# Kernel optimization log

Hardware: AMD Instinct MI355X
Metric: run time of the kernel (lower is better)

## Reference

```python
import jax, jax.numpy as jnp
import numpy as np

B, L, D = 8, 2048, 512


def setup_inputs() -> dict:
    key = jax.random.key(0)
    ks = jax.random.split(key, 9)
    s = 1.0 / np.sqrt(D)
    x = jax.random.normal(ks[0], (B, L, D), dtype=jnp.float32)
    Wq = jax.random.uniform(ks[1], (D, D), jnp.float32, -s, s)
    bq = jax.random.uniform(ks[2], (D,), jnp.float32, -s, s)
    Wk = jax.random.uniform(ks[3], (D, D), jnp.float32, -s, s)
    bk = jax.random.uniform(ks[4], (D,), jnp.float32, -s, s)
    Wv = jax.random.uniform(ks[5], (D, D), jnp.float32, -s, s)
    bv = jax.random.uniform(ks[6], (D,), jnp.float32, -s, s)
    Wo = jax.random.uniform(ks[7], (D, D), jnp.float32, -s, s)
    bo = jax.random.uniform(ks[8], (D,), jnp.float32, -s, s)
    return {"x": x, "Wq": Wq, "bq": bq, "Wk": Wk, "bk": bk,
            "Wv": Wv, "bv": bv, "Wo": Wo, "bo": bo}


def reference(x, Wq, bq, Wk, bk, Wv, bv, Wo, bo):
    # Projections then rfft along sequence axis -> complex [B, F, D], F = L//2+1
    Q = jnp.fft.rfft(x @ Wq + bq, axis=1)
    K = jnp.fft.rfft(x @ Wk + bk, axis=1)
    V = jnp.fft.rfft(x @ Wv + bv, axis=1)
    scale = K.shape[-1] ** (-0.5)
    # Complex attention scores over frequency bins: [B, F, F]
    att = jnp.einsum('bfd,bgd->bfg', Q, K) * scale
    attn = jax.nn.softmax(jnp.abs(att), axis=-1)
    context = jnp.einsum('bfg,bgd->bfd', attn.astype(Q.dtype), V)
    context = jnp.fft.irfft(context, n=x.shape[1], axis=1)  # [B, L, D] real
    return context @ Wo + bo
```

## Files before the change

kernel.cpp:

```cpp
#include <hip/hip_runtime.h>
#include <hip/hip_bf16.h>
#include <math.h>

typedef __hip_bfloat16 bf16;
typedef __attribute__((ext_vector_type(8))) short short8;
typedef __attribute__((ext_vector_type(4))) float f32x4;

#define BB 8
#define LL 2048
#define DD 512
#define FF 1025
#define GP 1088
#define FPAD 1152
#define PSTRIDE 589824
#define ATT_SCALE 0.04419417382415922f

__device__ __forceinline__ float b2f(bf16 v) { return __bfloat162float(v); }
__device__ __forceinline__ bf16  f2b(float v) { return __float2bfloat16(v); }
__device__ __forceinline__ float s2f(short s) { bf16 t; *reinterpret_cast<short*>(&t) = s; return b2f(t); }
__device__ __forceinline__ void splt(float v, short& h, short& l) {
    bf16 hb = f2b(v);
    bf16 lb = f2b(v - b2f(hb));
    h = *reinterpret_cast<short*>(&hb);
    l = *reinterpret_cast<short*>(&lb);
}
__device__ __forceinline__ unsigned pk2(short a, short b) {
    return (unsigned)(unsigned short)a | ((unsigned)(unsigned short)b << 16);
}

#define MFMA16(a, b, c) __builtin_amdgcn_mfma_f32_16x16x32_bf16((a), (b), (c), 0, 0, 0)

__device__ __forceinline__ short8 neg8(short8 v) {
    short8 r;
    #pragma unroll
    for (int t = 0; t < 8; ++t) r[t] = (short)(v[t] ^ (short)0x8000);
    return r;
}

typedef __attribute__((address_space(1))) const unsigned int gu32;
typedef __attribute__((address_space(3))) unsigned int lu32;
__device__ __forceinline__ void gl16(const void* g, void* l) {
    __builtin_amdgcn_global_load_lds((gu32*)g, (lu32*)l, 16, 0, 0);
}

template<bool F32>
__device__ __forceinline__ float ldin(const void* p, size_t i) {
    if (F32) return ((const float*)p)[i];
    else     return b2f(((const bf16*)p)[i]);
}

__global__ __launch_bounds__(256) void detect_dtype(const unsigned short* __restrict__ x,
                                                    int* __restrict__ flag)
{
    __shared__ int cnt[256];
    int c = 0;
    for (int i = threadIdx.x; i < 4096; i += 256) {
        const int e = (x[i] >> 7) & 0xFF;
        c += (e >= 100 && e <= 150) ? 1 : 0;
    }
    cnt[threadIdx.x] = c;
    __syncthreads();
    for (int s = 128; s; s >>= 1) {
        if (threadIdx.x < s) cnt[threadIdx.x] += cnt[threadIdx.x + s];
        __syncthreads();
    }
    if (threadIdx.x == 0) *flag = (cnt[0] < 3400) ? 1 : 0;
}

__global__ __launch_bounds__(256) void prep_bias(const void* __restrict__ b0,
                                                 const void* __restrict__ b1,
                                                 const void* __restrict__ b2,
                                                 const void* __restrict__ b3,
                                                 float* __restrict__ bias_f,
                                                 const int* __restrict__ flag)
{
    const int idx = blockIdx.x * 256 + threadIdx.x;
    const int which = idx >> 9, i = idx & 511;
    const void* src = which == 0 ? b0 : (which == 1 ? b1 : (which == 2 ? b2 : b3));
    bias_f[idx] = (*flag) ? ldin<true>(src, i) : ldin<false>(src, i);
}

__global__ __launch_bounds__(256) void split_w_t(const void* __restrict__ W0,
                                                 const void* __restrict__ W1,
                                                 const void* __restrict__ W2,
                                                 const void* __restrict__ W3,
                                                 bf16* __restrict__ WT,
                                                 const int* __restrict__ flag)
{
    const int z = blockIdx.z;
    const void* W = z == 0 ? W0 : (z == 1 ? W1 : (z == 2 ? W2 : W3));
    bf16* Wh = WT + (size_t)z * 524288;
    bf16* Wl = Wh + 262144;
    const int k0 = blockIdx.x * 32, n0 = blockIdx.y * 32;
    const bool f32 = (*flag) != 0;
    __shared__ float Tl[32][33];
    for (int it = 0; it < 4; ++it) {
        const int idx = it * 256 + threadIdx.x;
        const int lk = idx >> 5, ln = idx & 31;
        Tl[lk][ln] = f32 ? ldin<true>(W, (size_t)(k0 + lk) * 512 + n0 + ln)
                         : ldin<false>(W, (size_t)(k0 + lk) * 512 + n0 + ln);
    }
    __syncthreads();
    for (int it = 0; it < 4; ++it) {
        const int idx = it * 256 + threadIdx.x;
        const int ln = idx >> 5, lk = idx & 31;
        const float v = Tl[lk][ln];
        const bf16 h = f2b(v);
        Wh[(size_t)(n0 + ln) * 512 + k0 + lk] = h;
        Wl[(size_t)(n0 + ln) * 512 + k0 + lk] = f2b(v - b2f(h));
    }
}

__device__ __forceinline__ int shx(int i, int c) {
    const int x = (i << 2) | c;
    return x ^ (((x >> 6) & 3) << 2);
}

__device__ __forceinline__ void fft_decode(int flat, int& b, int& dp) {
    const int c8 = flat & 7;
    const int s  = (flat >> 3) & 1;
    const int pp = flat >> 4;
    const int idx = c8 * 32 + pp;
    b  = idx >> 5;
    dp = ((idx & 31) << 1) | s;
}

__global__ __launch_bounds__(512) void rfft_x(const void* __restrict__ x,
                                              bf16* __restrict__ Xh,
                                              bf16* __restrict__ Xl,
                                              const int* __restrict__ flag)
{
    int b, dp;
    fft_decode(blockIdx.x, b, dp);
    const int d0 = dp * 8;
    __shared__ float2 sh[8192];
    const int tid = threadIdx.x;
    const int c = tid & 3;

    if (*flag) {
        const float* base = (const float*)x + (size_t)b * 2048 * 512 + d0;
        #pragma unroll
        for (int it = 0; it < 8; ++it) {
            const int idx = it * 512 + tid;
            const int l = idx >> 1, fq = idx & 1;
            const float4 v = *(const float4*)(base + (size_t)l * 512 + fq * 4);
            sh[shx(l, fq * 2)]     = make_float2(v.x, v.y);
            sh[shx(l, fq * 2 + 1)] = make_float2(v.z, v.w);
        }
    } else {
        const bf16* base = (const bf16*)x + (size_t)b * 2048 * 512 + d0;
        #pragma unroll
        for (int it = 0; it < 4; ++it) {
            const int l = it * 512 + tid;
            const short8 v = *(const short8*)(base + (size_t)l * 512);
            #pragma unroll
            for (int q = 0; q < 4; ++q)
                sh[shx(l, q)] = make_float2(s2f(v[2 * q]), s2f(v[2 * q + 1]));
        }
    }
    __syncthreads();

    const int jb = tid >> 2;
    #pragma unroll
    for (int lsm = 10; lsm >= 0; --lsm) {
        const int m = 1 << lsm;
        const float step = -3.14159265358979f / (float)m;
        #pragma unroll
        for (int r = 0; r < 8; ++r) {
            const int j  = jb + 128 * r;
            const int k  = j & (m - 1);
            const int i1 = ((j & ~(m - 1)) << 1) | k;
            const int i2 = i1 + m;
            float sw, cw;
            __sincosf(step * (float)k, &sw, &cw);
            const float2 a  = sh[shx(i1, c)];
            const float2 bb = sh[shx(i2, c)];
            sh[shx(i1, c)] = make_float2(a.x + bb.x, a.y + bb.y);
            const float dx = a.x - bb.x, dy = a.y - bb.y;
            sh[shx(i2, c)] = make_float2(dx * cw - dy * sw, dx * sw + dy * cw);
        }
        __syncthreads();
    }

    const int fb = tid >> 2;
    const size_t pan_re = (size_t)(b * 64 + dp) * FPAD;
    const size_t pan_im = pan_re + (size_t)512 * FPAD;
    auto dorow = [&](int f) {
        const int rf = __brev((unsigned)f) >> 21;
        const int rc = __brev((unsigned)((2048 - f) & 2047)) >> 21;
        const float2 Zf = sh[shx(rf, c)];
        const float2 Zc = sh[shx(rc, c)];
        const float x1r = 0.5f * (Zf.x + Zc.x);
        const float x1i = 0.5f * (Zf.y - Zc.y);
        const float x2r = 0.5f * (Zf.y + Zc.y);
        const float x2i = -0.5f * (Zf.x - Zc.x);
        short h1r, l1r, h1i, l1i, h2r, l2r, h2i, l2i;
        splt(x1r, h1r, l1r); splt(x1i, h1i, l1i);
        splt(x2r, h2r, l2r); splt(x2i, h2i, l2i);
        const size_t ro_re = (pan_re + f) * 8 + 2 * c;
        const size_t ro_im = (pan_im + f) * 8 + 2 * c;
        *(unsigned*)&Xh[ro_re] = pk2(h1r, h2r);
        *(unsigned*)&Xh[ro_im] = pk2(h1i, h2i);
        *(unsigned*)&Xl[ro_re] = pk2(l1r, l2r);
        *(unsigned*)&Xl[ro_im] = pk2(l1i, l2i);
    };
    #pragma unroll
    for (int it = 0; it < 8; ++it)
        dorow(fb * 8 + it);
    if (tid < 4) dorow(1024);

    if (tid < 508) {
        const int f = FF + (tid >> 2);
        const int w = tid & 3;
        bf16* basep = (w & 2) ? Xl : Xh;
        const size_t off = (((size_t)((w & 1) * 512 + b * 64 + dp)) * FPAD + f) * 8;
        short8 z = {};
        *(short8*)&basep[off] = z;
    }
}

__global__ __launch_bounds__(256) void proj_all(const bf16* __restrict__ Xh,
                                                const bf16* __restrict__ Xl,
                                                const bf16* __restrict__ WT,
                                                const float* __restrict__ bias_f,
                                                bf16* __restrict__ Q,
                                                bf16* __restrict__ K,
                                                bf16* __restrict__ Vct)
{
    const int flat = blockIdx.x;
    const bool isV = flat < 576;
    int t, ny, z = 0;
    if (isV) { t = flat >> 2; ny = flat & 3; }
    else { const int idx = flat - 576; t = idx >> 3; z = (idx >> 2) & 1; ny = idx & 3; }

    const int pb = t / 9;
    const int f0 = (t - pb * 9) * 128;
    const int plane = pb >> 3, b = pb & 7;
    const int n0 = ny * 128;
    const int tid = threadIdx.x, wv = tid >> 6, lane = tid & 63;
    const int wm = (wv >> 1) * 64, wn = (wv & 1) * 64;
    const size_t pbase = (size_t)pb * PSTRIDE;

    __shared__ __align__(16) bf16 SH[16384];

    const int srow = tid >> 2, sq = tid & 3;
    const int mm = lane & 15, cc = lane >> 4;
    const int rpos = (cc ^ ((mm >> 1) & 3)) * 8;
    const int nn2 = lane & 15, rq = (lane >> 4) * 4;

    if (!isV) {
        const bf16* Bh = WT + (size_t)z * 524288;
        bf16* dst = z == 0 ? Q : K;
        const float* bias = bias_f + z * 512;
        typedef bf16 (*t128)[32];
        t128 Al = (t128)SH;
        t128 Bl = (t128)(SH + 4096);

        f32x4 acc[4][4] = {};
        for (int kt = 0; kt < 512; kt += 32) {
            #pragma unroll
            for (int p = 0; p < 2; ++p) {
                const int r = p * 64 + srow;
                const int pos = (sq ^ ((r >> 1) & 3)) * 8;
                *(uint4*)&Al[r][pos] =
                    *(const uint4*)&Xh[pbase + ((size_t)((kt >> 3) + sq) * FPAD + f0 + r) * 8];
                *(uint4*)&Bl[r][pos] = *(const uint4*)&Bh[(size_t)(n0 + r) * 512 + kt + sq * 8];
            }
            __syncthreads();

            short8 af[4], bfr[4];
            #pragma unroll
            for (int i = 0; i < 4; ++i) {
                af[i]  = *(const short8*)&Al[wm + i * 16 + mm][rpos];
                bfr[i] = *(const short8*)&Bl[wn + i * 16 + mm][rpos];
            }
            #pragma unroll
            for (int i = 0; i < 4; ++i)
                #pragma unroll
                for (int j = 0; j < 4; ++j)
                    acc[i][j] = MFMA16(af[i], bfr[j], acc[i][j]);
            __syncthreads();
        }

        const size_t SPQ = (size_t)BB * FF * DD;
        #pragma unroll
        for (int i = 0; i < 4; ++i)
            #pragma unroll
            for (int j = 0; j < 4; ++j) {
                const int col = n0 + wn + j * 16 + nn2;
                #pragma unroll
                for (int r = 0; r < 4; ++r) {
                    const int f = f0 + wm + i * 16 + rq + r;
                    if (f < FF) {
                        float v = acc[i][j][r];
                        if (plane == 0 && f == 0) v += 2048.0f * bias[col];
                        const int swz = ((f >> 1) & 3) << 3;
                        dst[(size_t)plane * SPQ + ((size_t)(b * FF + f)) * 512 + (col ^ swz)] = f2b(v);
                    }
                }
            }
    } else {
        const bf16* Bh = WT + (size_t)2 * 524288;
        const bf16* Blo = Bh + 262144;
        const float* bias = bias_f + 1024;
        typedef bf16 (*tile_t)[128][32];
        tile_t Al = (tile_t)SH;
        tile_t Bl = (tile_t)(SH + 8192);

        f32x4 acc[4][4] = {};
        for (int kt = 0; kt < 512; kt += 32) {
            #pragma unroll
            for (int p = 0; p < 2; ++p) {
                const int r = p * 64 + srow;
                const int pos = (sq ^ ((r >> 1) & 3)) * 8;
                const size_t aoff = pbase + ((size_t)((kt >> 3) + sq) * FPAD + f0 + r) * 8;
                *(uint4*)&Al[0][r][pos] = *(const uint4*)&Xh[aoff];
                *(uint4*)&Al[1][r][pos] = *(const uint4*)&Xl[aoff];
                *(uint4*)&Bl[0][r][pos] = *(const uint4*)&Bh[(size_t)(n0 + r) * 512 + kt + sq * 8];
                *(uint4*)&Bl[1][r][pos] = *(const uint4*)&Blo[(size_t)(n0 + r) * 512 + kt + sq * 8];
            }
            __syncthreads();

            short8 a_h[4], a_l[4], b_h[4], b_l[4];
            #pragma unroll
            for (int i = 0; i < 4; ++i) {
                a_h[i] = *(const short8*)&Al[0][wm + i * 16 + mm][rpos];
                a_l[i] = *(const short8*)&Al[1][wm + i * 16 + mm][rpos];
                b_h[i] = *(const short8*)&Bl[0][wn + i * 16 + mm][rpos];
                b_l[i] = *(const short8*)&Bl[1][wn + i * 16 + mm][rpos];
            }
            #pragma unroll
            for (int i = 0; i < 4; ++i)
                #pragma unroll
                for (int j = 0; j < 4; ++j) {
                    acc[i][j] = MFMA16(a_h[i], b_h[j], acc[i][j]);
                    acc[i][j] = MFMA16(a_h[i], b_l[j], acc[i][j]);
                    acc[i][j] = MFMA16(a_l[i], b_h[j], acc[i][j]);
                }
            __syncthreads();
        }

        bf16* T = SH;
        #pragma unroll
        for (int i = 0; i < 4; ++i)
            #pragma unroll
            for (int j = 0; j < 4; ++j) {
                const int col_l = wn + j * 16 + nn2;
                #pragma unroll
                for (int r = 0; r < 4; ++r) {
                    const int row_l = wm + i * 16 + rq + r;
                    const int f = f0 + row_l;
                    float v = (f < FF) ? acc[i][j][r] : 0.f;
                    if (plane == 0 && f == 0) v += 2048.0f * bias[n0 + col_l];
                    T[col_l * 128 + (row_l ^ ((col_l & 15) << 3))] = f2b(v);
                }
            }
        __syncthreads();

        const int nl = tid >> 1, half = tid & 1;
        const size_t gbase = ((size_t)(b * 1024 + plane * 512 + n0 + nl)) * GP + f0;
        #pragma unroll
        for (int a = 0; a < 8; ++a) {
            const int fl = half * 64 + a * 8;
            if (f0 + fl < GP) {
                const short8 v8 = *(const short8*)&T[nl * 128 + (fl ^ ((nl & 15) << 3))];
                *(short8*)&Vct[gbase + fl] = v8;
            }
        }
    }
}

__global__ __launch_bounds__(256, 2) void att_mfma(const bf16* __restrict__ Asp,
                                                   const bf16* __restrict__ Bsp,
                                                   float* __restrict__ att)
{
    const size_t SP = (size_t)BB * FF * DD;
    const int flat = blockIdx.x;
    const int b    = flat & 7;
    const int slot = flat >> 3;
    const int grp  = slot / 51;
    const int rem  = slot % 51;
    const int g    = rem / 3;
    const int r3   = rem % 3;
    const int ft   = grp * 3 + r3;
    const int f0 = ft * 128, g0 = g * 64;

    const int tid = threadIdx.x;
    const int wv = tid >> 6, lane = tid & 63;
    const int wvf = wv >> 1, wvg = wv & 1;

    __shared__ __align__(1024) char LB[24576];
    bf16 (*Al)[128][32] = (bf16(*)[128][32])LB;
    bf16 (*Bl)[64][32]  = (bf16(*)[64][32])(LB + 16384);

    f32x4 accr[4][2] = {}; f32x4 acci[4][2] = {};

    const int r16 = lane & 15, cc = lane >> 4;
    const int rpos = (cc ^ ((r16 >> 1) & 3)) * 8;
    const size_t abase = (size_t)(b * FF + f0) * 512;
    const size_t bbase = (size_t)(b * FF + g0) * 512;
    const int lrow = lane >> 2;
    const int lcol = (lane & 3) * 8;

    for (int kt = 0; kt < 512; kt += 32) {
        #pragma unroll
        for (int c2 = 0; c2 < 4; ++c2) {
            const int chunk = wv * 4 + c2;
            const int pl = chunk >> 3, rg = chunk & 7;
            const int row = rg * 16 + lrow;
            gl16(&Asp[(size_t)pl * SP + abase + (size_t)row * 512 + kt + lcol],
                 LB + chunk * 1024);
        }
        #pragma unroll
        for (int c2 = 0; c2 < 2; ++c2) {
            const int chunk = wv * 2 + c2;
            const int pl = chunk >> 2, rg = chunk & 3;
            const int row = rg * 16 + lrow;
            gl16(&Bsp[(size_t)pl * SP + bbase + (size_t)row * 512 + kt + lcol],
                 LB + 16384 + chunk * 1024);
        }
        __syncthreads();

        short8 aA[4][2], bB[2][2], nb[2];
        #pragma unroll
        for (int i = 0; i < 4; ++i) {
            const int row = wvf * 64 + i * 16 + r16;
            #pragma unroll
            for (int pl = 0; pl < 2; ++pl)
                aA[i][pl] = *(const short8*)&Al[pl][row][rpos];
        }
        #pragma unroll
        for (int j = 0; j < 2; ++j) {
            const int row = wvg * 32 + j * 16 + r16;
            #pragma unroll
            for (int pl = 0; pl < 2; ++pl)
                bB[j][pl] = *(const short8*)&Bl[pl][row][rpos];
            nb[j] = neg8(bB[j][1]);
        }
        #pragma unroll
        for (int i = 0; i < 4; ++i)
            #pragma unroll
            for (int j = 0; j < 2; ++j) {
                accr[i][j] = MFMA16(aA[i][0], bB[j][0], accr[i][j]);
                accr[i][j] = MFMA16(aA[i][1], nb[j],    accr[i][j]);
                acci[i][j] = MFMA16(aA[i][0], bB[j][1], acci[i][j]);
                acci[i][j] = MFMA16(aA[i][1], bB[j][0], acci[i][j]);
            }
        __syncthreads();
    }

    const int rq = (lane >> 4) * 4;
    #pragma unroll
    for (int i = 0; i < 4; ++i)
        #pragma unroll
        for (int j = 0; j < 2; ++j)
            #pragma unroll
            for (int r = 0; r < 4; ++r) {
                const int f = f0 + wvf * 64 + i * 16 + rq + r;
                const int gg = g0 + wvg * 32 + j * 16 + r16;
                if (f < FF && gg < FF) {
                    const float ar = accr[i][j][r];
                    const float ai = acci[i][j][r];
                    att[((size_t)(b * FF + f)) * FF + gg] = ATT_SCALE * sqrtf(ar * ar + ai * ai);
                }
            }
}

__global__ __launch_bounds__(256) void softmax_rows(const float* __restrict__ att,
                                                    bf16* __restrict__ att16)
{
    const int row = blockIdx.x;
    const float* p = att + (size_t)row * FF;
    bf16* q = att16 + (size_t)row * GP;
    const int tid = threadIdx.x;
    const int lane = tid & 63, wid = tid >> 6;
    __shared__ float red[4];

    float m = -1e30f;
    for (int i = tid; i < FF; i += 256) m = fmaxf(m, p[i]);
    #pragma unroll
    for (int o = 32; o; o >>= 1) m = fmaxf(m, __shfl_down(m, o));
    if (lane == 0) red[wid] = m;
    __syncthreads();
    m = fmaxf(fmaxf(red[0], red[1]), fmaxf(red[2], red[3]));
    __syncthreads();

    float s = 0.f;
    for (int i = tid; i < FF; i += 256) s += expf(p[i] - m);
    #pragma unroll
    for (int o = 32; o; o >>= 1) s += __shfl_down(s, o);
    if (lane == 0) red[wid] = s;
    __syncthreads();
    s = red[0] + red[1] + red[2] + red[3];
    const float inv = 1.f / s;
    for (int i = tid; i < GP; i += 256)
        q[i] = f2b(i < FF ? expf(p[i] - m) * inv : 0.f);
}

__global__ __launch_bounds__(256, 2) void ctx_mfma(const bf16* __restrict__ att16,
                                                   const bf16* __restrict__ Vct,
                                                   bf16* __restrict__ Csp)
{
    const int flat = blockIdx.x;
    const int b    = flat & 7;
    const int slot = flat >> 3;
    const int ft   = slot >> 4;
    const int nt   = slot & 15;
    const int f0 = ft * 128, n0 = nt * 64;

    const int tid = threadIdx.x;
    const int wv = tid >> 6, lane = tid & 63;
    const int wvf = wv >> 1, wvg = wv & 1;

    __shared__ __align__(16) bf16 Al[128][64];
    __shared__ __align__(16) bf16 Bl[64][64];

    f32x4 acc[4][2] = {};
    const int srow8 = tid >> 3, sq8 = tid & 7;
    const int r16 = lane & 15, cc = lane >> 4;
    const int rpos = (cc ^ ((r16 >> 1) & 3)) * 8;

    for (int kt = 0; kt < GP; kt += 64) {
        #pragma unroll
        for (int p = 0; p < 4; ++p) {
            const int row = p * 32 + srow8;
            const int pos = (sq8 >> 2) * 32 + (((sq8 & 3) ^ ((row >> 1) & 3)) * 8);
            uint4 av = make_uint4(0, 0, 0, 0);
            if (f0 + row < FF)
                av = *(const uint4*)&att16[((size_t)(b * FF + f0 + row)) * GP + kt + sq8 * 8];
            *(uint4*)&Al[row][pos] = av;
        }
        #pragma unroll
        for (int p = 0; p < 2; ++p) {
            const int row = p * 32 + srow8;
            const int pos = (sq8 >> 2) * 32 + (((sq8 & 3) ^ ((row >> 1) & 3)) * 8);
            *(uint4*)&Bl[row][pos] =
                *(const uint4*)&Vct[((size_t)(b * 1024 + n0 + row)) * GP + kt + sq8 * 8];
        }
        __syncthreads();

        #pragma unroll
        for (int kk = 0; kk < 2; ++kk) {
            short8 aA[4], bB[2];
            #pragma unroll
            for (int i = 0; i < 4; ++i)
                aA[i] = *(const short8*)&Al[wvf * 64 + i * 16 + r16][kk * 32 + rpos];
            #pragma unroll
            for (int j = 0; j < 2; ++j)
                bB[j] = *(const short8*)&Bl[wvg * 32 + j * 16 + r16][kk * 32 + rpos];
            #pragma unroll
            for (int i = 0; i < 4; ++i)
                #pragma unroll
                for (int j = 0; j < 2; ++j)
                    acc[i][j] = MFMA16(aA[i], bB[j], acc[i][j]);
        }
        __syncthreads();
    }

    const int rq = (lane >> 4) * 4;
    #pragma unroll
    for (int i = 0; i < 4; ++i)
        #pragma unroll
        for (int j = 0; j < 2; ++j)
            #pragma unroll
            for (int r = 0; r < 4; ++r) {
                const int f = f0 + wvf * 64 + i * 16 + rq + r;
                const int n = n0 + wvg * 32 + j * 16 + r16;
                if (f < FF) {
                    const int d = n & 511, pl = n >> 9;
                    Csp[((size_t)(pl * 8 + b) * FPAD + f) * 512 + d] = f2b(acc[i][j][r]);
                }
            }
}

__global__ __launch_bounds__(256) void out_mfma_freq(const bf16* __restrict__ A,
                                                     const bf16* __restrict__ BhT,
                                                     float* __restrict__ CwR,
                                                     float* __restrict__ CwI)
{
    const int t = blockIdx.x;
    const int pb = t / 9;
    const int f0 = (t - pb * 9) * 128;
    const int plane = pb >> 3, b = pb & 7;
    const int m0 = t * 128, n0 = blockIdx.y * 64;
    const int tid = threadIdx.x, wv = tid >> 6, lane = tid & 63;
    const int wvf = wv >> 1, wvg = wv & 1;

    __shared__ __align__(16) bf16 Al[128][32];
    __shared__ __align__(16) bf16 Bl[64][32];

    f32x4 acc[4][2] = {};
    const int srow = tid >> 2, sq = tid & 3;
    const int r16 = lane & 15, cc = lane >> 4;
    const int rpos = (cc ^ ((r16 >> 1) & 3)) * 8;

    for (int kt = 0; kt < 512; kt += 32) {
        #pragma unroll
        for (int p = 0; p < 2; ++p) {
            const int r = p * 64 + srow;
            const int pos = (sq ^ ((r >> 1) & 3)) * 8;
            *(uint4*)&Al[r][pos] = *(const uint4*)&A[(size_t)(m0 + r) * 512 + kt + sq * 8];
        }
        {
            const int pos = (sq ^ ((srow >> 1) & 3)) * 8;
            *(uint4*)&Bl[srow][pos] = *(const uint4*)&BhT[(size_t)(n0 + srow) * 512 + kt + sq * 8];
        }
        __syncthreads();

        short8 af[4], bfr[2];
        #pragma unroll
        for (int i = 0; i < 4; ++i)
            af[i] = *(const short8*)&Al[wvf * 64 + i * 16 + r16][rpos];
        #pragma unroll
        for (int j = 0; j < 2; ++j)
            bfr[j] = *(const short8*)&Bl[wvg * 32 + j * 16 + r16][rpos];
        #pragma unroll
        for (int i = 0; i < 4; ++i)
            #pragma unroll
            for (int j = 0; j < 2; ++j)
                acc[i][j] = MFMA16(af[i], bfr[j], acc[i][j]);
        __syncthreads();
    }

    float* dst = plane ? CwI : CwR;
    const int nn2 = lane & 15, rq = (lane >> 4) * 4;
    #pragma unroll
    for (int i = 0; i < 4; ++i)
        #pragma unroll
        for (int j = 0; j < 2; ++j) {
            const int col = n0 + wvg * 32 + j * 16 + nn2;
            #pragma unroll
            for (int r = 0; r < 4; ++r) {
                const int f = f0 + wvf * 64 + i * 16 + rq + r;
                if (f < FF)
                    dst[((size_t)(b * FF + f)) * 512 + col] = acc[i][j][r];
            }
        }
}

__global__ __launch_bounds__(512) void irfft8(const float* __restrict__ CwR,
                                              const float* __restrict__ CwI,
                                              void* __restrict__ out,
                                              const float* __restrict__ bias_f,
                                              const int* __restrict__ flag)
{
    int b, dp;
    fft_decode(blockIdx.x, b, dp);
    const int d0 = dp * 8;
    __shared__ float2 sh[8192];
    const int tid = threadIdx.x;
    const int c = tid & 3, fb = tid >> 2;

    for (int it = 0; it < 9; ++it) {
        const int f = fb + 128 * it;
        if (f < FF) {
            const size_t off = ((size_t)(b * FF + f)) * 512 + d0 + 2 * c;
            const float2 vr = *(const float2*)(CwR + off);
            const float2 vi = *(const float2*)(CwI + off);
            float c1x = vr.x, c1y = vi.x, c2x = vr.y, c2y = vi.y;
            if (f == 0 || f == 1024) { c1y = 0.f; c2y = 0.f; }
            sh[shx(f, c)] = make_float2(c1x - c2y, c1y + c2x);
            if (f >= 1 && f <= 1023)
                sh[shx(2048 - f, c)] = make_float2(c1x + c2y, c2x - c1y);
        }
    }
    __syncthreads();

    const int jb = fb;
    #pragma unroll
    for (int lsm = 10; lsm >= 0; --lsm) {
        const int m = 1 << lsm;
        const float step = 3.14159265358979f / (float)m;
        #pragma unroll
        for (int r = 0; r < 8; ++r) {
            const int j  = jb + 128 * r;
            const int k  = j & (m - 1);
            const int i1 = ((j & ~(m - 1)) << 1) | k;
            const int i2 = i1 + m;
            float sw, cw;
            __sincosf(step * (float)k, &sw, &cw);
            const float2 a  = sh[shx(i1, c)];
            const float2 bb = sh[shx(i2, c)];
            sh[shx(i1, c)] = make_float2(a.x + bb.x, a.y + bb.y);
            const float dx = a.x - bb.x, dy = a.y - bb.y;
            sh[shx(i2, c)] = make_float2(dx * cw - dy * sw, dx * sw + dy * cw);
        }
        __syncthreads();
    }

    const float sc = 1.0f / 2048.0f;
    const float bo0 = bias_f[1536 + d0 + 2 * c];
    const float bo1 = bias_f[1536 + d0 + 2 * c + 1];
    const bool f32o = (*flag) != 0;
    const int lb = tid >> 2;
    #pragma unroll
    for (int it = 0; it < 16; ++it) {
        const int l  = lb * 16 + it;
        const int rl = __brev((unsigned)l) >> 21;
        const float2 z = sh[shx(rl, c)];
        const float o0 = z.x * sc + bo0;
        const float o1 = z.y * sc + bo1;
        const size_t off = ((size_t)(b * 2048 + l)) * 512 + d0 + 2 * c;
        if (f32o) {
            *(float2*)((float*)out + off) = make_float2(o0, o1);
        } else {
            __hip_bfloat162 h;
            h.x = f2b(o0); h.y = f2b(o1);
            *(__hip_bfloat162*)((bf16*)out + off) = h;
        }
    }
}

extern "C" void kernel_launch(void* const* d_in, const int* in_sizes, int n_in,
                              void* d_out, int out_size, void* d_ws, size_t ws_size,
                              hipStream_t stream)
{
    const void* x  = d_in[0];
    const void* Wq = d_in[1]; const void* bq = d_in[2];
    const void* Wk = d_in[3]; const void* bk = d_in[4];
    const void* Wv = d_in[5]; const void* bv = d_in[6];
    const void* Wo = d_in[7]; const void* bo = d_in[8];

    char* ws = (char*)d_ws;
    char* pA = ws;
    char* pB = pA + 33652736;
    char* pC = pB + 37748736;
    char* pD = pC + 17039360;
    char* pE = pD + 17039360;
    char* pW = pE + 17825792;

    float*  attn = (float*)pA;
    bf16*   Xh   = (bf16*)pB;
    bf16*   Xl   = (bf16*)(pB + 18874368);
    bf16*   att16= (bf16*)pB;
    bf16*   Csp  = (bf16*)(pB + 17843200);
    bf16*   Asp  = (bf16*)pC;
    bf16*   Bsp  = (bf16*)pD;
    float*  CwR  = (float*)pC;
    float*  CwI  = (float*)pD;
    bf16*   Vct  = (bf16*)pE;
    bf16*   WT   = (bf16*)pW;
    float*  bias_f = (float*)(pW + 4194304);
    int*    flag = (int*)(pW + 4194304 + 8192);

    detect_dtype<<<1, 256, 0, stream>>>((const unsigned short*)x, flag);
    prep_bias<<<8, 256, 0, stream>>>(bq, bk, bv, bo, bias_f, flag);
    split_w_t<<<dim3(16, 16, 4), 256, 0, stream>>>(Wq, Wk, Wv, Wo, WT, flag);
    rfft_x<<<dim3(512), 512, 0, stream>>>(x, Xh, Xl, flag);
    proj_all<<<dim3(1728), 256, 0, stream>>>(Xh, Xl, WT, bias_f, Asp, Bsp, Vct);
    att_mfma<<<dim3(1224), 256, 0, stream>>>(Asp, Bsp, attn);
    softmax_rows<<<dim3(BB * FF), 256, 0, stream>>>(attn, att16);
    ctx_mfma<<<dim3(1152), 256, 0, stream>>>(att16, Vct, Csp);
    out_mfma_freq<<<dim3(144, 8), 256, 0, stream>>>(Csp, WT + 3 * 524288, CwR, CwI);
    irfft8<<<dim3(512), 512, 0, stream>>>(CwR, CwI, d_out, bias_f, flag);
}
```

Baseline: 364.4 us.

## Precompute FFT twiddles in LDS, widen GEMM k-tile, cache softmax row in LDS

```diff
diff --git a/kernel.cpp b/kernel.cpp
--- a/kernel.cpp
+++ b/kernel.cpp
@@ -125,6 +125,17 @@
     dp = ((idx & 31) << 1) | s;
 }
 
+__device__ __forceinline__ void fill_twl(float2* twl, int tid) {
+    for (int idx = tid; idx < 2047; idx += 512) {
+        const int l2 = 31 - __builtin_clz((unsigned)(2047 - idx));
+        const int m = 1 << l2;
+        const int k = idx - 2048 + 2 * m;
+        float s, c2;
+        __sincosf(-3.14159265358979f * (float)k / (float)m, &s, &c2);
+        twl[idx] = make_float2(c2, s);
+    }
+}
+
 __global__ __launch_bounds__(512) void rfft_x(const void* __restrict__ x,
                                               bf16* __restrict__ Xh,
                                               bf16* __restrict__ Xl,
@@ -134,6 +145,7 @@
     fft_decode(blockIdx.x, b, dp);
     const int d0 = dp * 8;
     __shared__ float2 sh[8192];
+    __shared__ float2 twl[2048];
     const int tid = threadIdx.x;
     const int c = tid & 3;
 
@@ -158,21 +170,22 @@
                 sh[shx(l, q)] = make_float2(s2f(v[2 * q]), s2f(v[2 * q + 1]));
         }
     }
+    fill_twl(twl, tid);
     __syncthreads();
 
     const int jb = tid >> 2;
     #pragma unroll
     for (int lsm = 10; lsm >= 0; --lsm) {
         const int m = 1 << lsm;
-        const float step = -3.14159265358979f / (float)m;
+        const int base = 2048 - (m << 1);
         #pragma unroll
         for (int r = 0; r < 8; ++r) {
             const int j  = jb + 128 * r;
             const int k  = j & (m - 1);
             const int i1 = ((j & ~(m - 1)) << 1) | k;
             const int i2 = i1 + m;
-            float sw, cw;
-            __sincosf(step * (float)k, &sw, &cw);
+            const float2 w = twl[base + k];
+            const float cw = w.x, sw = w.y;
             const float2 a  = sh[shx(i1, c)];
             const float2 bb = sh[shx(i2, c)];
             sh[shx(i1, c)] = make_float2(a.x + bb.x, a.y + bb.y);
@@ -252,33 +265,38 @@
         const bf16* Bh = WT + (size_t)z * 524288;
         bf16* dst = z == 0 ? Q : K;
         const float* bias = bias_f + z * 512;
-        typedef bf16 (*t128)[32];
-        t128 Al = (t128)SH;
-        t128 Bl = (t128)(SH + 4096);
+        typedef bf16 (*t64)[64];
+        t64 Al = (t64)SH;
+        t64 Bl = (t64)(SH + 8192);
+        const int srow8 = tid >> 3, sq8 = tid & 7;
 
         f32x4 acc[4][4] = {};
-        for (int kt = 0; kt < 512; kt += 32) {
-            #pragma unroll
-            for (int p = 0; p < 2; ++p) {
-                const int r = p * 64 + srow;
-                const int pos = (sq ^ ((r >> 1) & 3)) * 8;
-                *(uint4*)&Al[r][pos] =
-                    *(const uint4*)&Xh[pbase + ((size_t)((kt >> 3) + sq) * FPAD + f0 + r) * 8];
-                *(uint4*)&Bl[r][pos] = *(const uint4*)&Bh[(size_t)(n0 + r) * 512 + kt + sq * 8];
+        for (int kt = 0; kt < 512; kt += 64) {
+            #pragma unroll
+            for (int p = 0; p < 4; ++p) {
+                const int row = p * 32 + srow8;
+                const int pos = (sq8 >> 2) * 32 + (((sq8 & 3) ^ ((row >> 1) & 3)) * 8);
+                *(uint4*)&Al[row][pos] =
+                    *(const uint4*)&Xh[pbase + ((size_t)((kt >> 3) + sq8) * FPAD + f0 + row) * 8];
+                *(uint4*)&Bl[row][pos] =
+                    *(const uint4*)&Bh[(size_t)(n0 + row) * 512 + kt + sq8 * 8];
             }
             __syncthreads();
 
-            short8 af[4], bfr[4];
-            #pragma unroll
-            for (int i = 0; i < 4; ++i) {
-                af[i]  = *(const short8*)&Al[wm + i * 16 + mm][rpos];
-                bfr[i] = *(const short8*)&Bl[wn + i * 16 + mm][rpos];
-            }
-            #pragma unroll
-            for (int i = 0; i < 4; ++i)
+            #pragma unroll
+            for (int kk = 0; kk < 2; ++kk) {
+                short8 af[4], bfr[4];
                 #pragma unroll
-                for (int j = 0; j < 4; ++j)
-                    acc[i][j] = MFMA16(af[i], bfr[j], acc[i][j]);
+                for (int i = 0; i < 4; ++i) {
+                    af[i]  = *(const short8*)&Al[wm + i * 16 + mm][kk * 32 + rpos];
+                    bfr[i] = *(const short8*)&Bl[wn + i * 16 + mm][kk * 32 + rpos];
+                }
+                #pragma unroll
+                for (int i = 0; i < 4; ++i)
+                    #pragma unroll
+                    for (int j = 0; j < 4; ++j)
+                        acc[i][j] = MFMA16(af[i], bfr[j], acc[i][j]);
+            }
             __syncthreads();
         }
 
@@ -474,10 +492,15 @@
     bf16* q = att16 + (size_t)row * GP;
     const int tid = threadIdx.x;
     const int lane = tid & 63, wid = tid >> 6;
+    __shared__ float srow[1028];
     __shared__ float red[4];
 
     float m = -1e30f;
-    for (int i = tid; i < FF; i += 256) m = fmaxf(m, p[i]);
+    for (int i = tid; i < FF; i += 256) {
+        const float v = p[i];
+        srow[i] = v;
+        m = fmaxf(m, v);
+    }
     #pragma unroll
     for (int o = 32; o; o >>= 1) m = fmaxf(m, __shfl_down(m, o));
     if (lane == 0) red[wid] = m;
@@ -486,7 +509,7 @@
     __syncthreads();
 
     float s = 0.f;
-    for (int i = tid; i < FF; i += 256) s += expf(p[i] - m);
+    for (int i = tid; i < FF; i += 256) s += expf(srow[i] - m);
     #pragma unroll
     for (int o = 32; o; o >>= 1) s += __shfl_down(s, o);
     if (lane == 0) red[wid] = s;
@@ -494,7 +517,7 @@
     s = red[0] + red[1] + red[2] + red[3];
     const float inv = 1.f / s;
     for (int i = tid; i < GP; i += 256)
-        q[i] = f2b(i < FF ? expf(p[i] - m) * inv : 0.f);
+        q[i] = f2b(i < FF ? expf(srow[i] - m) * inv : 0.f);
 }
 
 __global__ __launch_bounds__(256, 2) void ctx_mfma(const bf16* __restrict__ att16,
@@ -648,6 +671,7 @@
     fft_decode(blockIdx.x, b, dp);
     const int d0 = dp * 8;
     __shared__ float2 sh[8192];
+    __shared__ float2 twl[2048];
     const int tid = threadIdx.x;
     const int c = tid & 3, fb = tid >> 2;
 
@@ -664,21 +688,22 @@
                 sh[shx(2048 - f, c)] = make_float2(c1x + c2y, c2x - c1y);
         }
     }
+    fill_twl(twl, tid);
     __syncthreads();
 
     const int jb = fb;
     #pragma unroll
     for (int lsm = 10; lsm >= 0; --lsm) {
         const int m = 1 << lsm;
-        const float step = 3.14159265358979f / (float)m;
+        const int base = 2048 - (m << 1);
         #pragma unroll
         for (int r = 0; r < 8; ++r) {
             const int j  = jb + 128 * r;
             const int k  = j & (m - 1);
             const int i1 = ((j & ~(m - 1)) << 1) | k;
             const int i2 = i1 + m;
-            float sw, cw;
-            __sincosf(step * (float)k, &sw, &cw);
+            const float2 w = twl[base + k];
+            const float cw = w.x, sw = -w.y;
             const float2 a  = sh[shx(i1, c)];
             const float2 bb = sh[shx(i2, c)];
             sh[shx(i1, c)] = make_float2(a.x + bb.x, a.y + bb.y);
```

New measurement: 366.3 us. About the same (+0.5%).
